# Kernel optimization log

Hardware: AMD Instinct MI355X
Metric: run time of the kernel (lower is better)

Reference implementation:

```python
import jax, jax.numpy as jnp
import numpy as np

N_HEAD = 16
D_MODEL = 1024
D_K = D_MODEL // N_HEAD  # 64
LN_EPS = 1e-5


def setup_inputs() -> dict:
    key = jax.random.key(0)
    ks = jax.random.split(key, 12)
    B, L, D = 4, 2048, D_MODEL
    std_qkv = float(np.sqrt(2.0 / (D + D_K)))
    q = jax.random.normal(ks[0], (B, L, D), jnp.float32)
    k = jax.random.normal(ks[1], (B, L, D), jnp.float32)
    v = jax.random.normal(ks[2], (B, L, D), jnp.float32)
    Wq = jax.random.normal(ks[3], (D, D), jnp.float32) * std_qkv
    Wk = jax.random.normal(ks[4], (D, D), jnp.float32) * std_qkv
    Wv = jax.random.normal(ks[5], (D, D), jnp.float32) * std_qkv
    bq = jnp.zeros((D,), jnp.float32)
    bk = jnp.zeros((D,), jnp.float32)
    bv = jnp.zeros((D,), jnp.float32)
    # xavier normal for fc: std = sqrt(2/(fan_in+fan_out))
    Wo = jax.random.normal(ks[6], (D, D), jnp.float32) * float(np.sqrt(2.0 / (D + D)))
    bo = jnp.zeros((D,), jnp.float32)
    gamma = jnp.ones((D,), jnp.float32)
    beta = jnp.zeros((D,), jnp.float32)
    return {"q": q, "k": k, "v": v, "Wq": Wq, "bq": bq, "Wk": Wk, "bk": bk,
            "Wv": Wv, "bv": bv, "Wo": Wo, "bo": bo, "gamma": gamma, "beta": beta}


def _layer_norm(x, gamma, beta):
    mu = jnp.mean(x, axis=-1, keepdims=True)
    var = jnp.mean(jnp.square(x - mu), axis=-1, keepdims=True)
    return (x - mu) * jax.lax.rsqrt(var + LN_EPS) * gamma + beta


def reference(q, k, v, Wq, bq, Wk, bk, Wv, bv, Wo, bo, gamma, beta):
    B, Lq, D = q.shape
    Lk = k.shape[1]
    h, dk = N_HEAD, D_K
    residual = q
    # projections (torch Linear: x @ W.T + b), split heads -> (h, b, l, dk)
    qh = (q @ Wq.T + bq).reshape(B, Lq, h, dk).transpose(2, 0, 1, 3)
    kh = (k @ Wk.T + bk).reshape(B, Lk, h, dk).transpose(2, 0, 1, 3)
    vh = (v @ Wv.T + bv).reshape(B, Lk, h, dk).transpose(2, 0, 1, 3)
    temp = jnp.asarray(np.power(dk, 0.5), qh.dtype)
    scores = jnp.einsum('hbqd,hbkd->hbqk', qh, kh) / temp
    attn = jax.nn.softmax(scores, axis=-1)  # softmax over key dim (dim=2 of bmm view)
    out = jnp.einsum('hbqk,hbkd->hbqd', attn, vh)
    # (h,b,lq,dk) -> (b,lq,h*dk)
    out = out.transpose(1, 2, 0, 3).reshape(B, Lq, D)
    out = out @ Wo.T + bo  # dropout p=0.0 -> identity
    out = _layer_norm(out + residual, gamma, beta)
    attn_flat = attn.reshape(h * B, Lq, Lk)  # matches torch (n_head*sz_b, lq, lk)
    return out, attn_flat
```

## Files before the change

### kernel.cpp

```cpp
#include <hip/hip_runtime.h>
#include <stdint.h>

typedef short bf16x8 __attribute__((ext_vector_type(8)));
typedef float f32x4 __attribute__((ext_vector_type(4)));
typedef unsigned short us4 __attribute__((ext_vector_type(4)));
typedef unsigned short us8 __attribute__((ext_vector_type(8)));
typedef unsigned uint2v __attribute__((ext_vector_type(2)));

#define SCL 0.18033688011112042f

__device__ __forceinline__ unsigned short f2bf(float f) {
  union { float f; unsigned u; } v; v.f = f;
  unsigned r = v.u + 0x7fffu + ((v.u >> 16) & 1u);
  return (unsigned short)(r >> 16);
}

__device__ __forceinline__ unsigned cvtpk(float lo, float hi) {
  unsigned r;
  asm("v_cvt_pk_bf16_f32 %0, %1, %2" : "=v"(r) : "v"(lo), "v"(hi));
  return r;
}

__device__ __forceinline__ float bf2f(unsigned short h) {
  union { unsigned u; float f; } v; v.u = ((unsigned)h) << 16; return v.f;
}

#define GL2LDS(g, l) __builtin_amdgcn_global_load_lds( \
    (const __attribute__((address_space(1))) void*)(g), \
    (__attribute__((address_space(3))) void*)(l), 16, 0, 0)

__global__ __launch_bounds__(256) void convert_all(
    const float* __restrict__ q, const float* __restrict__ k, const float* __restrict__ v,
    const float* __restrict__ wq, const float* __restrict__ wk, const float* __restrict__ wv,
    const float* __restrict__ wo,
    unsigned short* __restrict__ qb, unsigned short* __restrict__ kb, unsigned short* __restrict__ vb,
    unsigned short* __restrict__ wqb, unsigned short* __restrict__ wkb, unsigned short* __restrict__ wvb,
    unsigned short* __restrict__ wob)
{
  const long NB = 8388608, NW = 1048576;
  long i = ((long)blockIdx.x * 256 + threadIdx.x) * 4;
  if (i >= 3*NB + 4*NW) return;
  const float* src; unsigned short* dst; long off;
  if (i < NB)              { src = q;  dst = qb;  off = i; }
  else if (i < 2*NB)       { src = k;  dst = kb;  off = i - NB; }
  else if (i < 3*NB)       { src = v;  dst = vb;  off = i - 2*NB; }
  else if (i < 3*NB+NW)    { src = wq; dst = wqb; off = i - 3*NB; }
  else if (i < 3*NB+2*NW)  { src = wk; dst = wkb; off = i - 3*NB - NW; }
  else if (i < 3*NB+3*NW)  { src = wv; dst = wvb; off = i - 3*NB - 2*NW; }
  else                     { src = wo; dst = wob; off = i - 3*NB - 3*NW; }
  float4 x = *(const float4*)(src + off);
  us4 o; o.x = f2bf(x.x); o.y = f2bf(x.y); o.z = f2bf(x.z); o.w = f2bf(x.w);
  *(us4*)(dst + off) = o;
}

__global__ __launch_bounds__(256, 2) void qkv_gemm(
    const unsigned short* __restrict__ qb, const unsigned short* __restrict__ kb,
    const unsigned short* __restrict__ vb,
    const unsigned short* __restrict__ wqb, const unsigned short* __restrict__ wkb,
    const unsigned short* __restrict__ wvb,
    const float* __restrict__ bq, const float* __restrict__ bk, const float* __restrict__ bv,
    unsigned short* __restrict__ qh, unsigned short* __restrict__ kh,
    unsigned short* __restrict__ vt)
{
  const int z = blockIdx.z;
  const unsigned short* X = (z == 0) ? qb : (z == 1) ? kb : vb;
  const unsigned short* W = (z == 0) ? wqb : (z == 1) ? wkb : wvb;
  const float* bias = (z == 0) ? bq : (z == 1) ? bk : bv;
  unsigned short* dqh = (z == 0) ? qh : kh;
  const float sc = (z == 0) ? SCL : 1.0f;

  const int flat = blockIdx.x + (blockIdx.y << 6);
  const int xcd = flat & 7, ii = flat >> 3;
  const int m0 = (xcd * 8 + (ii & 7)) * 128;
  const int n0 = (ii >> 3) * 128;

  const int tid = threadIdx.x, lane = tid & 63, w = tid >> 6;
  const int wr = w >> 1, wc = w & 1;
  const int lg = lane >> 4, ll = lane & 15;

  __shared__ __align__(16) unsigned short As[128 * 32];
  __shared__ __align__(16) unsigned short Bs[128 * 32];

  f32x4 acc[4][4] = {};

  const char* gA = (const char*)X + ((size_t)(m0 + w*32 + (lane >> 2)) * 1024) * 2 + (lane & 3) * 16;
  const char* gB = (const char*)W + ((size_t)(n0 + w*32 + (lane >> 2)) * 1024) * 2 + (lane & 3) * 16;
  char* lA = (char*)As + w * 2048;
  char* lB = (char*)Bs + w * 2048;

  for (int k0 = 0; k0 < 1024; k0 += 32) {
    GL2LDS(gA,         lA);
    GL2LDS(gA + 32768, lA + 1024);
    GL2LDS(gB,         lB);
    GL2LDS(gB + 32768, lB + 1024);
    gA += 64; gB += 64;
    __syncthreads();
    bf16x8 xa[4], wb[4];
    const int kc = lg * 8;
#pragma unroll
    for (int f = 0; f < 4; ++f) xa[f] = *(const bf16x8*)&As[(wr*64 + f*16 + ll)*32 + kc];
#pragma unroll
    for (int f = 0; f < 4; ++f) wb[f] = *(const bf16x8*)&Bs[(wc*64 + f*16 + ll)*32 + kc];
    if (z < 2) {
#pragma unroll
      for (int fn = 0; fn < 4; ++fn)
#pragma unroll
        for (int fm = 0; fm < 4; ++fm)
          acc[fn][fm] = __builtin_amdgcn_mfma_f32_16x16x32_bf16(wb[fn], xa[fm], acc[fn][fm], 0, 0, 0);
    } else {
#pragma unroll
      for (int fm = 0; fm < 4; ++fm)
#pragma unroll
        for (int fn = 0; fn < 4; ++fn)
          acc[fm][fn] = __builtin_amdgcn_mfma_f32_16x16x32_bf16(xa[fm], wb[fn], acc[fm][fn], 0, 0, 0);
    }
    __syncthreads();
  }

  if (z < 2) {
#pragma unroll
    for (int fn = 0; fn < 4; ++fn) {
      const int n_g = n0 + wc*64 + fn*16 + lg*4;
      const float4 b4 = *(const float4*)&bias[n_g];
      const int h = n_g >> 6, dkk = n_g & 63;
#pragma unroll
      for (int fm = 0; fm < 4; ++fm) {
        const int m_g = m0 + wr*64 + fm*16 + ll;
        const int b_ = m_g >> 11, l_ = m_g & 2047;
        us4 pk;
        pk.x = f2bf((acc[fn][fm][0] + b4.x) * sc);
        pk.y = f2bf((acc[fn][fm][1] + b4.y) * sc);
        pk.z = f2bf((acc[fn][fm][2] + b4.z) * sc);
        pk.w = f2bf((acc[fn][fm][3] + b4.w) * sc);
        *(us4*)&dqh[((size_t)(h*4 + b_) * 2048 + l_) * 64 + dkk] = pk;
      }
    }
  } else {
#pragma unroll
    for (int fn = 0; fn < 4; ++fn) {
      const int n_g = n0 + wc*64 + fn*16 + ll;
      const float bias_n = bias[n_g];
      const int h = n_g >> 6, dkk = n_g & 63;
#pragma unroll
      for (int fm = 0; fm < 4; ++fm) {
        const int mrow = m0 + wr*64 + fm*16 + lg*4;
        const int b_ = mrow >> 11, l_ = mrow & 2047;
        us4 pk;
        pk.x = f2bf(acc[fm][fn][0] + bias_n);
        pk.y = f2bf(acc[fm][fn][1] + bias_n);
        pk.z = f2bf(acc[fm][fn][2] + bias_n);
        pk.w = f2bf(acc[fm][fn][3] + bias_n);
        *(us4*)&vt[((size_t)(h*4 + b_) * 64 + dkk) * 2048 + l_] = pk;
      }
    }
  }
}

__global__ __launch_bounds__(256, 2) void attn_kernel(
    const unsigned short* __restrict__ qh, const unsigned short* __restrict__ kh,
    const unsigned short* __restrict__ vt, float* __restrict__ probs,
    unsigned short* __restrict__ attn_o)
{
  const int bid = blockIdx.x;
  const int xcd = bid & 7;
  const int idx = bid >> 3;
  const int hb  = xcd * 8 + (idx & 7);
  const int qt  = idx >> 3;

  const int tid = threadIdx.x, lane = tid & 63, w = tid >> 6;
  const int wr = w >> 1, wc = w & 1;
  const int lg = lane >> 4, ll = lane & 15;

  __shared__ __align__(16) char smem[33792];
  unsigned short* Pb = (unsigned short*)smem;
  float* rs   = (float*)(smem + 18432);
  float* invl = (float*)(smem + 19456);
  float* Ored = (float*)smem;

  const size_t slab = (size_t)hb << 17;

  bf16x8 qf[4][2];
#pragma unroll
  for (int fq = 0; fq < 4; ++fq)
#pragma unroll
    for (int dh = 0; dh < 2; ++dh)
      qf[fq][dh] = *(const bf16x8*)&qh[slab + (size_t)(qt*128 + wr*64 + fq*16 + ll)*64 + dh*32 + lg*8];

  const unsigned short* Kf = kh + slab + (size_t)(wc*32 + ll)*64 + lg*8;
  const unsigned short* Vf = vt + slab + (size_t)ll*2048 + wc*32 + lg*8;

  float rsum[4] = {0.f, 0.f, 0.f, 0.f};
  for (int kt = 0; kt < 32; ++kt) {
    bf16x8 ka[2][2];
#pragma unroll
    for (int fk = 0; fk < 2; ++fk)
#pragma unroll
      for (int dh = 0; dh < 2; ++dh)
        ka[fk][dh] = *(const bf16x8*)(Kf + kt*4096 + fk*1024 + dh*32);
    f32x4 s[2][4] = {};
    __builtin_amdgcn_s_setprio(1);
#pragma unroll
    for (int dh = 0; dh < 2; ++dh)
#pragma unroll
      for (int fk = 0; fk < 2; ++fk)
#pragma unroll
        for (int fq = 0; fq < 4; ++fq)
          s[fk][fq] = __builtin_amdgcn_mfma_f32_16x16x32_bf16(ka[fk][dh], qf[fq][dh], s[fk][fq], 0, 0, 0);
    __builtin_amdgcn_s_setprio(0);
#pragma unroll
    for (int fk = 0; fk < 2; ++fk)
#pragma unroll
      for (int fq = 0; fq < 4; ++fq)
#pragma unroll
        for (int r = 0; r < 4; ++r)
          rsum[fq] += exp2f(s[fk][fq][r]);
  }

#pragma unroll
  for (int fq = 0; fq < 4; ++fq) {
    float t = rsum[fq];
    t += __shfl_xor(t, 16);
    t += __shfl_xor(t, 32);
    rsum[fq] = t;
  }
  if (lg == 0) {
#pragma unroll
    for (int fq = 0; fq < 4; ++fq)
      rs[wc*128 + wr*64 + fq*16 + ll] = rsum[fq];
  }
  __syncthreads();
  if (tid < 128) invl[tid] = 1.0f / (rs[tid] + rs[128 + tid]);
  __syncthreads();
  float inv_r[4];
#pragma unroll
  for (int fq = 0; fq < 4; ++fq) inv_r[fq] = invl[wr*64 + fq*16 + ll];

  f32x4 o[4][4] = {};
  float* pb2 = probs + ((size_t)hb << 22) + (size_t)(qt*128) * 2048;
  const int prow = tid >> 4, pcol = (tid & 15) * 4;

  auto body = [&](bf16x8 (&ka)[2][2], bf16x8 (&kan)[2][2], int kt) {
    bf16x8 vb[4];
#pragma unroll
    for (int f = 0; f < 4; ++f)
      vb[f] = *(const bf16x8*)(Vf + f*32768 + kt*64);

    f32x4 s[2][4] = {};
    __builtin_amdgcn_s_setprio(1);
#pragma unroll
    for (int dh = 0; dh < 2; ++dh)
#pragma unroll
      for (int fk = 0; fk < 2; ++fk)
#pragma unroll
        for (int fq = 0; fq < 4; ++fq)
          s[fk][fq] = __builtin_amdgcn_mfma_f32_16x16x32_bf16(ka[fk][dh], qf[fq][dh], s[fk][fq], 0, 0, 0);
    __builtin_amdgcn_s_setprio(0);

    if (kt + 1 < 32) {
#pragma unroll
      for (int fk = 0; fk < 2; ++fk)
#pragma unroll
        for (int dh = 0; dh < 2; ++dh)
          kan[fk][dh] = *(const bf16x8*)(Kf + (kt+1)*4096 + fk*1024 + dh*32);
    }

#pragma unroll
    for (int fk = 0; fk < 2; ++fk)
#pragma unroll
      for (int fq = 0; fq < 4; ++fq) {
        float p0 = exp2f(s[fk][fq][0]) * inv_r[fq];
        float p1 = exp2f(s[fk][fq][1]) * inv_r[fq];
        float p2 = exp2f(s[fk][fq][2]) * inv_r[fq];
        float p3 = exp2f(s[fk][fq][3]) * inv_r[fq];
        uint2v u; u.x = cvtpk(p0, p1); u.y = cvtpk(p2, p3);
        *(uint2v*)&Pb[(wr*64 + fq*16 + ll)*72 + wc*32 + fk*16 + lg*4] = u;
      }
    __syncthreads();

    float* pdst = pb2 + kt*64;
#pragma unroll
    for (int j = 0; j < 8; ++j) {
      const int row = j*16 + prow;
      us4 pv = *(const us4*)&Pb[row*72 + pcol];
      f32x4 pf; pf[0] = bf2f(pv.x); pf[1] = bf2f(pv.y); pf[2] = bf2f(pv.z); pf[3] = bf2f(pv.w);
      __builtin_nontemporal_store(pf, (f32x4*)(pdst + (size_t)row*2048 + pcol));
    }

    bf16x8 pa[4];
#pragma unroll
    for (int fm = 0; fm < 4; ++fm)
      pa[fm] = *(const bf16x8*)&Pb[(wr*64 + fm*16 + ll)*72 + wc*32 + lg*8];
    __builtin_amdgcn_s_setprio(1);
#pragma unroll
    for (int fm = 0; fm < 4; ++fm)
#pragma unroll
      for (int fd = 0; fd < 4; ++fd)
        o[fm][fd] = __builtin_amdgcn_mfma_f32_16x16x32_bf16(pa[fm], vb[fd], o[fm][fd], 0, 0, 0);
    __builtin_amdgcn_s_setprio(0);
    __syncthreads();
  };

  bf16x8 kaA[2][2], kaB[2][2];
#pragma unroll
  for (int fk = 0; fk < 2; ++fk)
#pragma unroll
    for (int dh = 0; dh < 2; ++dh)
      kaA[fk][dh] = *(const bf16x8*)(Kf + fk*1024 + dh*32);
  for (int kt = 0; kt < 32; kt += 2) {
    body(kaA, kaB, kt);
    body(kaB, kaA, kt + 1);
  }

  if (wc == 1) {
#pragma unroll
    for (int fm = 0; fm < 4; ++fm)
#pragma unroll
      for (int fd = 0; fd < 4; ++fd)
#pragma unroll
        for (int r = 0; r < 4; ++r)
          Ored[wr*4096 + (fm*16 + lg*4 + r)*64 + fd*16 + ll] = o[fm][fd][r];
  }
  __syncthreads();
  if (wc == 0) {
    const int b_ = hb & 3, h = hb >> 2;
#pragma unroll
    for (int fm = 0; fm < 4; ++fm)
#pragma unroll
      for (int fd = 0; fd < 4; ++fd)
#pragma unroll
        for (int r = 0; r < 4; ++r) {
          const int qrow = fm*16 + lg*4 + r;
          const int d = fd*16 + ll;
          float val = o[fm][fd][r] + Ored[wr*4096 + qrow*64 + d];
          const int mg = b_*2048 + qt*128 + wr*64 + qrow;
          attn_o[(size_t)mg*1024 + h*64 + d] = f2bf(val);
        }
  }
}

__global__ __launch_bounds__(256, 2) void outproj_gemm(
    const unsigned short* __restrict__ Ain, const unsigned short* __restrict__ Wob,
    const float* __restrict__ bo, const float* __restrict__ qres, float* __restrict__ preLN)
{
  const int flat = blockIdx.x + (blockIdx.y << 6);
  const int xcd = flat & 7, ii = flat >> 3;
  const int m0 = (xcd * 8 + (ii & 7)) * 128;
  const int n0 = (ii >> 3) * 128;

  const int tid = threadIdx.x, lane = tid & 63, w = tid >> 6;
  const int wr = w >> 1, wc = w & 1;
  const int lg = lane >> 4, ll = lane & 15;

  __shared__ __align__(16) unsigned short As[128 * 32];
  __shared__ __align__(16) unsigned short Bs[128 * 32];

  f32x4 acc[4][4] = {};

  const char* gA = (const char*)Ain + ((size_t)(m0 + w*32 + (lane >> 2)) * 1024) * 2 + (lane & 3) * 16;
  const char* gB = (const char*)Wob + ((size_t)(n0 + w*32 + (lane >> 2)) * 1024) * 2 + (lane & 3) * 16;
  char* lA = (char*)As + w * 2048;
  char* lB = (char*)Bs + w * 2048;

  for (int k0 = 0; k0 < 1024; k0 += 32) {
    GL2LDS(gA,         lA);
    GL2LDS(gA + 32768, lA + 1024);
    GL2LDS(gB,         lB);
    GL2LDS(gB + 32768, lB + 1024);
    gA += 64; gB += 64;
    __syncthreads();
    bf16x8 xa[4], wb[4];
    const int kc = lg * 8;
#pragma unroll
    for (int f = 0; f < 4; ++f) xa[f] = *(const bf16x8*)&As[(wr*64 + f*16 + ll)*32 + kc];
#pragma unroll
    for (int f = 0; f < 4; ++f) wb[f] = *(const bf16x8*)&Bs[(wc*64 + f*16 + ll)*32 + kc];
#pragma unroll
    for (int fn = 0; fn < 4; ++fn)
#pragma unroll
      for (int fm = 0; fm < 4; ++fm)
        acc[fn][fm] = __builtin_amdgcn_mfma_f32_16x16x32_bf16(wb[fn], xa[fm], acc[fn][fm], 0, 0, 0);
    __syncthreads();
  }

#pragma unroll
  for (int fn = 0; fn < 4; ++fn) {
    const int n_g = n0 + wc*64 + fn*16 + lg*4;
    const float4 b4 = *(const float4*)&bo[n_g];
#pragma unroll
    for (int fm = 0; fm < 4; ++fm) {
      const int m_g = m0 + wr*64 + fm*16 + ll;
      const size_t idxp = (size_t)m_g * 1024 + n_g;
      const float4 r4 = *(const float4*)&qres[idxp];
      f32x4 y;
      y[0] = acc[fn][fm][0] + b4.x + r4.x;
      y[1] = acc[fn][fm][1] + b4.y + r4.y;
      y[2] = acc[fn][fm][2] + b4.z + r4.z;
      y[3] = acc[fn][fm][3] + b4.w + r4.w;
      *(f32x4*)&preLN[idxp] = y;
    }
  }
}

__global__ __launch_bounds__(256) void ln_kernel(
    const float* __restrict__ x, const float* __restrict__ gamma,
    const float* __restrict__ beta, float* __restrict__ out)
{
  const int row = blockIdx.x, tid = threadIdx.x;
  const float4 xv = ((const float4*)(x + (size_t)row * 1024))[tid];
  float s = xv.x + xv.y + xv.z + xv.w;
  float ss = xv.x*xv.x + xv.y*xv.y + xv.z*xv.z + xv.w*xv.w;
#pragma unroll
  for (int m = 1; m < 64; m <<= 1) { s += __shfl_xor(s, m); ss += __shfl_xor(ss, m); }
  __shared__ float red[8];
  if ((tid & 63) == 0) { red[(tid >> 6)*2] = s; red[(tid >> 6)*2 + 1] = ss; }
  __syncthreads();
  s  = red[0] + red[2] + red[4] + red[6];
  ss = red[1] + red[3] + red[5] + red[7];
  const float mu = s * (1.0f/1024.0f);
  const float var = ss * (1.0f/1024.0f) - mu*mu;
  const float rstd = rsqrtf(var + 1e-5f);
  const float4 g  = ((const float4*)gamma)[tid];
  const float4 be = ((const float4*)beta)[tid];
  float4 y;
  y.x = (xv.x - mu)*rstd*g.x + be.x;
  y.y = (xv.y - mu)*rstd*g.y + be.y;
  y.z = (xv.z - mu)*rstd*g.z + be.z;
  y.w = (xv.w - mu)*rstd*g.w + be.w;
  ((float4*)(out + (size_t)row * 1024))[tid] = y;
}

extern "C" void kernel_launch(void* const* d_in, const int* in_sizes, int n_in,
                              void* d_out, int out_size, void* d_ws, size_t ws_size,
                              hipStream_t stream) {
  const float* q     = (const float*)d_in[0];
  const float* k     = (const float*)d_in[1];
  const float* v     = (const float*)d_in[2];
  const float* Wq    = (const float*)d_in[3];
  const float* bq    = (const float*)d_in[4];
  const float* Wk    = (const float*)d_in[5];
  const float* bk    = (const float*)d_in[6];
  const float* Wv    = (const float*)d_in[7];
  const float* bv    = (const float*)d_in[8];
  const float* Wo    = (const float*)d_in[9];
  const float* bo    = (const float*)d_in[10];
  const float* gamma = (const float*)d_in[11];
  const float* beta  = (const float*)d_in[12];

  float* out   = (float*)d_out;
  float* probs = out + 8388608;

  char* ws = (char*)d_ws;
  unsigned short* qb  = (unsigned short*)(ws);
  unsigned short* kb  = (unsigned short*)(ws + 16777216);
  unsigned short* vb  = (unsigned short*)(ws + 33554432);
  unsigned short* wqb = (unsigned short*)(ws + 50331648);
  unsigned short* wkb = (unsigned short*)(ws + 52428800);
  unsigned short* wvb = (unsigned short*)(ws + 54525952);
  unsigned short* wob = (unsigned short*)(ws + 56623104);
  unsigned short* qh  = (unsigned short*)(ws + 58720256);
  unsigned short* kh  = (unsigned short*)(ws + 75497472);
  unsigned short* vt  = (unsigned short*)(ws + 92274688);
  float* preLN = (float*)(ws);
  unsigned short* attn_o = vb;

  convert_all<<<28672, 256, 0, stream>>>(q, k, v, Wq, Wk, Wv, Wo,
                                         qb, kb, vb, wqb, wkb, wvb, wob);

  dim3 g1(64, 8, 3);
  qkv_gemm<<<g1, 256, 0, stream>>>(qb, kb, vb, wqb, wkb, wvb, bq, bk, bv, qh, kh, vt);

  attn_kernel<<<1024, 256, 0, stream>>>(qh, kh, vt, probs, attn_o);

  dim3 g3(64, 8);
  outproj_gemm<<<g3, 256, 0, stream>>>(attn_o, wob, bo, q, preLN);

  ln_kernel<<<8192, 256, 0, stream>>>(preLN, gamma, beta, out);
}
```

Before: 445.9 us.

## Double-buffer LDS tiles in GEMMs and the P tile in attention

The QKV and output-projection GEMMs now ping-pong between two LDS stages. The next K-slice is issued with global-to-LDS loads before computing on the current slice, which removes the load-then-barrier stall at the top of each iteration. The attention kernel double-buffers its bf16 probability tile, drops one barrier per key tile, and moves the fp32 probs write-out after the PV MFMAs so that the store traffic overlaps the matrix math. The cost is more LDS per block, which may limit occupancy, and a final barrier before the output reduction reuses shared memory.

```diff
diff --git a/kernel.cpp b/kernel.cpp
--- a/kernel.cpp
+++ b/kernel.cpp
@@ -78,29 +78,35 @@
   const int wr = w >> 1, wc = w & 1;
   const int lg = lane >> 4, ll = lane & 15;
 
-  __shared__ __align__(16) unsigned short As[128 * 32];
-  __shared__ __align__(16) unsigned short Bs[128 * 32];
+  __shared__ __align__(16) unsigned short As[2 * 128 * 32];
+  __shared__ __align__(16) unsigned short Bs[2 * 128 * 32];
 
   f32x4 acc[4][4] = {};
 
   const char* gA = (const char*)X + ((size_t)(m0 + w*32 + (lane >> 2)) * 1024) * 2 + (lane & 3) * 16;
   const char* gB = (const char*)W + ((size_t)(n0 + w*32 + (lane >> 2)) * 1024) * 2 + (lane & 3) * 16;
-  char* lA = (char*)As + w * 2048;
-  char* lB = (char*)Bs + w * 2048;
+
+#define STAGE_G(buf) do { \
+    char* lA_ = (char*)As + (buf)*8192 + w*2048; \
+    char* lB_ = (char*)Bs + (buf)*8192 + w*2048; \
+    GL2LDS(gA, lA_); GL2LDS(gA + 32768, lA_ + 1024); \
+    GL2LDS(gB, lB_); GL2LDS(gB + 32768, lB_ + 1024); \
+    gA += 64; gB += 64; } while (0)
+
+  STAGE_G(0);
+  __syncthreads();
 
   for (int k0 = 0; k0 < 1024; k0 += 32) {
-    GL2LDS(gA,         lA);
-    GL2LDS(gA + 32768, lA + 1024);
-    GL2LDS(gB,         lB);
-    GL2LDS(gB + 32768, lB + 1024);
-    gA += 64; gB += 64;
-    __syncthreads();
+    const int cur = (k0 >> 5) & 1;
+    if (k0 < 992) STAGE_G(cur ^ 1);
+    const unsigned short* Ac = As + cur * 4096;
+    const unsigned short* Bc = Bs + cur * 4096;
     bf16x8 xa[4], wb[4];
     const int kc = lg * 8;
 #pragma unroll
-    for (int f = 0; f < 4; ++f) xa[f] = *(const bf16x8*)&As[(wr*64 + f*16 + ll)*32 + kc];
-#pragma unroll
-    for (int f = 0; f < 4; ++f) wb[f] = *(const bf16x8*)&Bs[(wc*64 + f*16 + ll)*32 + kc];
+    for (int f = 0; f < 4; ++f) xa[f] = *(const bf16x8*)&Ac[(wr*64 + f*16 + ll)*32 + kc];
+#pragma unroll
+    for (int f = 0; f < 4; ++f) wb[f] = *(const bf16x8*)&Bc[(wc*64 + f*16 + ll)*32 + kc];
     if (z < 2) {
 #pragma unroll
       for (int fn = 0; fn < 4; ++fn)
@@ -171,10 +177,10 @@
   const int wr = w >> 1, wc = w & 1;
   const int lg = lane >> 4, ll = lane & 15;
 
-  __shared__ __align__(16) char smem[33792];
+  __shared__ __align__(16) char smem[38400];
   unsigned short* Pb = (unsigned short*)smem;
-  float* rs   = (float*)(smem + 18432);
-  float* invl = (float*)(smem + 19456);
+  float* rs   = (float*)(smem + 36864);
+  float* invl = (float*)(smem + 37888);
   float* Ored = (float*)smem;
 
   const size_t slab = (size_t)hb << 17;
@@ -240,6 +246,7 @@
   const int prow = tid >> 4, pcol = (tid & 15) * 4;
 
   auto body = [&](bf16x8 (&ka)[2][2], bf16x8 (&kan)[2][2], int kt) {
+    unsigned short* Pc = Pb + (kt & 1) * 9216;
     bf16x8 vb[4];
 #pragma unroll
     for (int f = 0; f < 4; ++f)
@@ -273,23 +280,14 @@
         float p2 = exp2f(s[fk][fq][2]) * inv_r[fq];
         float p3 = exp2f(s[fk][fq][3]) * inv_r[fq];
         uint2v u; u.x = cvtpk(p0, p1); u.y = cvtpk(p2, p3);
-        *(uint2v*)&Pb[(wr*64 + fq*16 + ll)*72 + wc*32 + fk*16 + lg*4] = u;
+        *(uint2v*)&Pc[(wr*64 + fq*16 + ll)*72 + wc*32 + fk*16 + lg*4] = u;
       }
     __syncthreads();
 
-    float* pdst = pb2 + kt*64;
-#pragma unroll
-    for (int j = 0; j < 8; ++j) {
-      const int row = j*16 + prow;
-      us4 pv = *(const us4*)&Pb[row*72 + pcol];
-      f32x4 pf; pf[0] = bf2f(pv.x); pf[1] = bf2f(pv.y); pf[2] = bf2f(pv.z); pf[3] = bf2f(pv.w);
-      __builtin_nontemporal_store(pf, (f32x4*)(pdst + (size_t)row*2048 + pcol));
-    }
-
     bf16x8 pa[4];
 #pragma unroll
     for (int fm = 0; fm < 4; ++fm)
-      pa[fm] = *(const bf16x8*)&Pb[(wr*64 + fm*16 + ll)*72 + wc*32 + lg*8];
+      pa[fm] = *(const bf16x8*)&Pc[(wr*64 + fm*16 + ll)*72 + wc*32 + lg*8];
     __builtin_amdgcn_s_setprio(1);
 #pragma unroll
     for (int fm = 0; fm < 4; ++fm)
@@ -297,7 +295,15 @@
       for (int fd = 0; fd < 4; ++fd)
         o[fm][fd] = __builtin_amdgcn_mfma_f32_16x16x32_bf16(pa[fm], vb[fd], o[fm][fd], 0, 0, 0);
     __builtin_amdgcn_s_setprio(0);
-    __syncthreads();
+
+    float* pdst = pb2 + kt*64;
+#pragma unroll
+    for (int j = 0; j < 8; ++j) {
+      const int row = j*16 + prow;
+      us4 pv = *(const us4*)&Pc[row*72 + pcol];
+      f32x4 pf; pf[0] = bf2f(pv.x); pf[1] = bf2f(pv.y); pf[2] = bf2f(pv.z); pf[3] = bf2f(pv.w);
+      __builtin_nontemporal_store(pf, (f32x4*)(pdst + (size_t)row*2048 + pcol));
+    }
   };
 
   bf16x8 kaA[2][2], kaB[2][2];
@@ -311,6 +317,7 @@
     body(kaB, kaA, kt + 1);
   }
 
+  __syncthreads();
   if (wc == 1) {
 #pragma unroll
     for (int fm = 0; fm < 4; ++fm)
@@ -351,29 +358,28 @@
   const int wr = w >> 1, wc = w & 1;
   const int lg = lane >> 4, ll = lane & 15;
 
-  __shared__ __align__(16) unsigned short As[128 * 32];
-  __shared__ __align__(16) unsigned short Bs[128 * 32];
+  __shared__ __align__(16) unsigned short As[2 * 128 * 32];
+  __shared__ __align__(16) unsigned short Bs[2 * 128 * 32];
 
   f32x4 acc[4][4] = {};
 
   const char* gA = (const char*)Ain + ((size_t)(m0 + w*32 + (lane >> 2)) * 1024) * 2 + (lane & 3) * 16;
   const char* gB = (const char*)Wob + ((size_t)(n0 + w*32 + (lane >> 2)) * 1024) * 2 + (lane & 3) * 16;
-  char* lA = (char*)As + w * 2048;
-  char* lB = (char*)Bs + w * 2048;
+
+  STAGE_G(0);
+  __syncthreads();
 
   for (int k0 = 0; k0 < 1024; k0 += 32) {
-    GL2LDS(gA,         lA);
-    GL2LDS(gA + 32768, lA + 1024);
-    GL2LDS(gB,         lB);
-    GL2LDS(gB + 32768, lB + 1024);
-    gA += 64; gB += 64;
-    __syncthreads();
+    const int cur = (k0 >> 5) & 1;
+    if (k0 < 992) STAGE_G(cur ^ 1);
+    const unsigned short* Ac = As + cur * 4096;
+    const unsigned short* Bc = Bs + cur * 4096;
     bf16x8 xa[4], wb[4];
     const int kc = lg * 8;
 #pragma unroll
-    for (int f = 0; f < 4; ++f) xa[f] = *(const bf16x8*)&As[(wr*64 + f*16 + ll)*32 + kc];
-#pragma unroll
-    for (int f = 0; f < 4; ++f) wb[f] = *(const bf16x8*)&Bs[(wc*64 + f*16 + ll)*32 + kc];
+    for (int f = 0; f < 4; ++f) xa[f] = *(const bf16x8*)&Ac[(wr*64 + f*16 + ll)*32 + kc];
+#pragma unroll
+    for (int f = 0; f < 4; ++f) wb[f] = *(const bf16x8*)&Bc[(wc*64 + f*16 + ll)*32 + kc];
 #pragma unroll
     for (int fn = 0; fn < 4; ++fn)
 #pragma unroll
```

New measurement: 443.6 us. No clear change (-0.5%).
